# Optimization experiments

Measured on AMD Instinct MI355X. Metric: run time of the kernel, lower is better.

## Reference

```python
import jax, jax.numpy as jnp
import numpy as np
from jax import lax

IN_CH, OUT_CH, K, STYLE_DIM = 512, 512, 3, 512
B, H, W = 16, 64, 64
SCALE = 1.0 / np.sqrt(IN_CH * K * K).astype(np.float32)
EPS = 1e-8


def setup_inputs() -> dict:
    key = jax.random.key(0)
    k1, k2, k3, k4 = jax.random.split(key, 4)
    return {
        "x": jax.random.normal(k1, (B, IN_CH, H, W), dtype=jnp.float32),
        "style": jax.random.normal(k2, (B, STYLE_DIM), dtype=jnp.float32),
        "weight": jax.random.normal(k3, (1, OUT_CH, IN_CH, K, K), dtype=jnp.float32),
        "mod_w": jax.random.normal(k4, (IN_CH, STYLE_DIM), dtype=jnp.float32) / np.sqrt(STYLE_DIM),
        "mod_b": jnp.ones((IN_CH,), dtype=jnp.float32),
    }


def reference(x, style, weight, mod_w, mod_b):
    b, cin, h, w = x.shape
    out_ch = weight.shape[1]
    k = weight.shape[-1]
    pad = k // 2
    # style projection: (B, in_channel)
    s = style @ mod_w.T + mod_b
    # modulated weight: (B, out, in, k, k)
    wmod = SCALE * weight * s[:, None, :, None, None]
    # demodulation: rsqrt of sum of squares over (in, kh, kw)
    demod = lax.rsqrt(jnp.sum(wmod * wmod, axis=(2, 3, 4)) + EPS)
    wmod = wmod * demod[:, :, None, None, None]
    # grouped conv with groups = batch
    wflat = wmod.reshape(b * out_ch, cin, k, k)
    xin = x.reshape(1, b * cin, h, w)
    out = lax.conv_general_dilated(
        xin, wflat,
        window_strides=(1, 1),
        padding=[(pad, pad), (pad, pad)],
        dimension_numbers=("NCHW", "OIHW", "NCHW"),
        feature_group_count=b,
    )
    return out.reshape(b, out_ch, h, w)
```

## Files before the change

kernel.cpp:

```cpp
#include <hip/hip_runtime.h>
#include <hip/hip_bf16.h>
#include <cstdint>
#include <cstddef>

typedef __bf16 bf16x8 __attribute__((ext_vector_type(8)));
typedef float f32x4 __attribute__((ext_vector_type(4)));

#define MOD_SCALE 1.4731391e-02f
#define EPSF 1e-8f

__global__ __launch_bounds__(512) void k_style(
    const float* __restrict__ style, const float* __restrict__ mod_w,
    const float* __restrict__ mod_b, float* __restrict__ s)
{
  __shared__ float st[512];
  const int b = blockIdx.x, i = threadIdx.x;
  st[i] = style[b*512 + i];
  __syncthreads();
  const float4* mw = (const float4*)(mod_w + (size_t)i*512);
  float acc = 0.f;
  #pragma unroll 8
  for (int j = 0; j < 128; ++j) {
    float4 v = mw[j];
    acc += v.x*st[4*j] + v.y*st[4*j+1] + v.z*st[4*j+2] + v.w*st[4*j+3];
  }
  s[b*512 + i] = acc + mod_b[i];
}

__global__ __launch_bounds__(256) void k_weight(
    const float* __restrict__ weight, float* __restrict__ w2,
    __hip_bfloat16* __restrict__ Wb)
{
  const int o = blockIdx.x, t = threadIdx.x;
  #pragma unroll
  for (int h = 0; h < 2; ++h) {
    const int i = t + h*256;
    const float* wp = weight + ((size_t)o*512 + i)*9;
    float sq = 0.f;
    #pragma unroll
    for (int kk = 0; kk < 9; ++kk) {
      float v = wp[kk];
      sq += v*v;
      Wb[((size_t)kk*512 + o)*512 + i] = __float2bfloat16(v * MOD_SCALE);
    }
    w2[(size_t)o*512 + i] = sq;
  }
}

__global__ __launch_bounds__(256) void k_demod(
    const float* __restrict__ s, const float* __restrict__ w2,
    float* __restrict__ demod)
{
  __shared__ float s2[512];
  const int b = blockIdx.x, t = threadIdx.x;
  {
    float a = s[b*512 + t];        s2[t]     = a*a;
    float c = s[b*512 + t + 256];  s2[t+256] = c*c;
  }
  __syncthreads();
  #pragma unroll
  for (int h = 0; h < 2; ++h) {
    const int o = t + h*256;
    const float4* wp = (const float4*)(w2 + (size_t)o*512);
    float acc = 0.f;
    #pragma unroll 8
    for (int j = 0; j < 128; ++j) {
      float4 v = wp[j];
      acc += v.x*s2[4*j] + v.y*s2[4*j+1] + v.z*s2[4*j+2] + v.w*s2[4*j+3];
    }
    demod[b*512 + o] = rsqrtf(MOD_SCALE*MOD_SCALE*acc + EPSF);
  }
}

__global__ __launch_bounds__(256) void k_xm(
    const float* __restrict__ x, const float* __restrict__ s,
    __hip_bfloat16* __restrict__ Xm)
{
  __shared__ __hip_bfloat16 T[64][40];
  const int bid = blockIdx.x;
  const int cb = bid & 15, y = (bid >> 4) & 63, b = bid >> 10;
  const int ic0 = cb*32;
  const int t = threadIdx.x;
  const int i = t >> 3, x0 = (t & 7)*8;
  const float sv = s[b*512 + ic0 + i];
  const float4* xp = (const float4*)(x + (size_t)(b*512 + ic0 + i)*4096 + y*64 + x0);
  float4 v0 = xp[0], v1 = xp[1];
  float vals[8] = {v0.x, v0.y, v0.z, v0.w, v1.x, v1.y, v1.z, v1.w};
  #pragma unroll
  for (int j = 0; j < 8; ++j) T[x0+j][i] = __float2bfloat16(vals[j]*sv);
  __syncthreads();
  const int p = t >> 2, c = (t & 3)*8;
  __hip_bfloat16* dst = Xm + (((size_t)(b*66 + (y+1))*66 + (p+1))*512 + ic0 + c);
  *(float4*)dst = *(const float4*)&T[p][c];
}

#define VMC(n) asm volatile("s_waitcnt vmcnt(" #n ")" ::: "memory")

__global__ __launch_bounds__(512, 2) void k_conv(
    const __hip_bfloat16* __restrict__ Wb,
    const __hip_bfloat16* __restrict__ Xm,
    const float* __restrict__ demod,
    float* __restrict__ out)
{
  __shared__ __hip_bfloat16 lds[2][2][16384];

  const int orig = blockIdx.x;
  const int swz = (orig & 7)*64 + (orig >> 3);
  const int b  = swz >> 5;
  const int nt = (swz & 31) >> 1;
  const int mt = swz & 1;
  const int o0 = mt*256, y0 = nt*4;

  const int tid = threadIdx.x;
  const int l = tid & 63;
  const int w = tid >> 6;
  const int wm = w >> 2;
  const int wn = w & 3;

  const int srow = tid >> 3;
  const int scol = ((tid & 7) << 4) ^ ((srow & 7) << 4);
  const char* WbC = (const char*)Wb;
  const char* XmC = (const char*)Xm;

  const int frow = l & 15;
  const int fk0 = ((l >> 4) << 4) ^ ((l & 7) << 4);
  const int fk1 = fk0 ^ 64;
  const int aRow0 = (wm*64 + frow)*128;
  const int bRow0 = (wn*32 + frow)*128;

  #define STAGE_A(tau, h, bfi) do { \
    const int kk_ = (tau) >> 3; \
    const int cb_ = ((tau) & 7) << 7; \
    _Pragma("unroll") \
    for (int it_ = 0; it_ < 2; ++it_) { \
      const int orow_ = o0 + (h)*128 + it_*64 + srow; \
      const char* src_ = WbC + (size_t)(kk_*512 + orow_)*1024 + cb_ + scol; \
      __builtin_amdgcn_global_load_lds( \
        (__attribute__((address_space(1))) void*)src_, \
        (__attribute__((address_space(3))) void*)((char*)&lds[bfi][0][0] + (h)*16384 + it_*8192 + w*1024), \
        16, 0, 0); \
    } \
  } while(0)

  #define STAGE_B(tau, h, bfi) do { \
    const int kk_ = (tau) >> 3; \
    const int cb_ = ((tau) & 7) << 7; \
    const int dy_ = kk_/3 - 1, dx_ = kk_ - (kk_/3)*3 - 1; \
    _Pragma("unroll") \
    for (int it_ = 0; it_ < 2; ++it_) { \
      const int py_ = y0 + (h)*2 + it_ + dy_ + 1; \
      const int px_ = srow + dx_ + 1; \
      const char* src_ = XmC + ((size_t)((b*66 + py_)*66 + px_))*1024 + cb_ + scol; \
      __builtin_amdgcn_global_load_lds( \
        (__attribute__((address_space(1))) void*)src_, \
        (__attribute__((address_space(3))) void*)((char*)&lds[bfi][1][0] + (h)*16384 + it_*8192 + w*1024), \
        16, 0, 0); \
    } \
  } while(0)

  #define RD_A(Ab, MH) do { \
    _Pragma("unroll") \
    for (int mi_ = 0; mi_ < 4; ++mi_) { \
      a_[mi_][0] = *(const bf16x8*)((Ab) + aRow0 + (MH)*16384 + mi_*2048 + fk0); \
      a_[mi_][1] = *(const bf16x8*)((Ab) + aRow0 + (MH)*16384 + mi_*2048 + fk1); \
    } \
  } while(0)

  #define RD_B(Bb, NH) do { \
    _Pragma("unroll") \
    for (int ni_ = 0; ni_ < 2; ++ni_) { \
      b_[ni_][0] = *(const bf16x8*)((Bb) + bRow0 + (NH)*16384 + ni_*2048 + fk0); \
      b_[ni_][1] = *(const bf16x8*)((Bb) + bRow0 + (NH)*16384 + ni_*2048 + fk1); \
    } \
  } while(0)

  #define MFMAQ(MH, NH) do { \
    _Pragma("unroll") \
    for (int mi_ = 0; mi_ < 4; ++mi_) \
      _Pragma("unroll") \
      for (int ni_ = 0; ni_ < 2; ++ni_) { \
        acc[(MH)*4+mi_][(NH)*2+ni_] = __builtin_amdgcn_mfma_f32_16x16x32_bf16( \
            a_[mi_][0], b_[ni_][0], acc[(MH)*4+mi_][(NH)*2+ni_], 0, 0, 0); \
        acc[(MH)*4+mi_][(NH)*2+ni_] = __builtin_amdgcn_mfma_f32_16x16x32_bf16( \
            a_[mi_][1], b_[ni_][1], acc[(MH)*4+mi_][(NH)*2+ni_], 0, 0, 0); \
      } \
  } while(0)

  #define TILE(BFI, S1, S2, S3, S4, VM2, VM4) do { \
    const char* Ab_ = (const char*)&lds[BFI][0][0]; \
    const char* Bb_ = (const char*)&lds[BFI][1][0]; \
    bf16x8 a_[4][2], b_[2][2]; \
     \
    RD_A(Ab_, 0); RD_B(Bb_, 0); \
    S1; \
    __builtin_amdgcn_s_barrier(); \
    __builtin_amdgcn_s_setprio(1); MFMAQ(0, 0); __builtin_amdgcn_s_setprio(0); \
    __builtin_amdgcn_s_barrier(); \
     \
    RD_A(Ab_, 1); \
    S2; \
    __builtin_amdgcn_s_barrier(); \
    __builtin_amdgcn_s_setprio(1); MFMAQ(1, 0); __builtin_amdgcn_s_setprio(0); \
    VM2; \
    __builtin_amdgcn_s_barrier(); \
     \
    RD_B(Bb_, 1); \
    S3; \
    __builtin_amdgcn_s_barrier(); \
    __builtin_amdgcn_s_setprio(1); MFMAQ(1, 1); __builtin_amdgcn_s_setprio(0); \
    __builtin_amdgcn_s_barrier(); \
     \
    RD_A(Ab_, 0); \
    S4; \
    __builtin_amdgcn_s_barrier(); \
    __builtin_amdgcn_s_setprio(1); MFMAQ(0, 1); __builtin_amdgcn_s_setprio(0); \
    VM4; \
    __builtin_amdgcn_s_barrier(); \
  } while(0)

  f32x4 acc[8][4] = {};

  STAGE_A(0, 0, 0); STAGE_A(0, 1, 0); STAGE_B(0, 0, 0); STAGE_B(0, 1, 0);
  STAGE_B(1, 0, 1); STAGE_A(1, 1, 1);
  VMC(4);
  __builtin_amdgcn_s_barrier();

  #pragma unroll 1
  for (int tt = 0; tt < 35; ++tt) {
    const int t = tt*2;
    TILE(0, STAGE_A(t+1,0,1), STAGE_B(t+1,1,1), STAGE_B(t+2,0,0), STAGE_A(t+2,1,0),
            VMC(8), VMC(6));
    TILE(1, STAGE_A(t+2,0,0), STAGE_B(t+2,1,0), STAGE_B(t+3,0,1), STAGE_A(t+3,1,1),
            VMC(8), VMC(6));
  }
  TILE(0, STAGE_A(71,0,1), STAGE_B(71,1,1), (void)0, (void)0, VMC(8), VMC(2));
  TILE(1, (void)0, (void)0, (void)0, (void)0, VMC(0), (void)0);

  #pragma unroll
  for (int m = 0; m < 8; ++m) {
    const int o = o0 + wm*64 + (m >> 2)*128 + (m & 3)*16 + ((l >> 4) << 2);
    const f32x4 dm = *(const f32x4*)(demod + b*512 + o);
    #pragma unroll
    for (int n = 0; n < 4; ++n) {
      const int nc = wn*32 + (n >> 1)*128 + (n & 1)*16 + (l & 15);
      const int y = y0 + (nc >> 6), xx = nc & 63;
      float* op = out + (size_t)(b*512 + o)*4096 + y*64 + xx;
      #pragma unroll
      for (int r = 0; r < 4; ++r)
        op[(size_t)r*4096] = acc[m][n][r]*dm[r];
    }
  }
  #undef TILE
  #undef MFMAQ
  #undef RD_A
  #undef RD_B
  #undef STAGE_A
  #undef STAGE_B
}

extern "C" void kernel_launch(void* const* d_in, const int* in_sizes, int n_in,
                              void* d_out, int out_size, void* d_ws, size_t ws_size,
                              hipStream_t stream)
{
  const float* x      = (const float*)d_in[0];
  const float* style  = (const float*)d_in[1];
  const float* weight = (const float*)d_in[2];
  const float* mod_w  = (const float*)d_in[3];
  const float* mod_b  = (const float*)d_in[4];
  float* out = (float*)d_out;

  char* ws = (char*)d_ws;
  float* s            = (float*)(ws);
  float* demod        = (float*)(ws + 32768);
  float* w2           = (float*)(ws + 65536);
  __hip_bfloat16* Wb  = (__hip_bfloat16*)(ws + 1114112);
  __hip_bfloat16* Xm  = (__hip_bfloat16*)(ws + 5832704);

  hipMemsetAsync(Xm, 0, (size_t)16*66*66*512*2, stream);

  k_style <<<16,    512, 0, stream>>>(style, mod_w, mod_b, s);
  k_weight<<<512,   256, 0, stream>>>(weight, w2, Wb);
  k_demod <<<16,    256, 0, stream>>>(s, w2, demod);
  k_xm    <<<16384, 256, 0, stream>>>(x, s, Xm);
  k_conv  <<<512,   512, 0, stream>>>(Wb, Xm, demod, out);
}
```

Before: 397.1 us.

## Switch conv MFMA to 32x32x16 tiles and zero Xm halo in k_xm

```diff
diff --git a/kernel.cpp b/kernel.cpp
--- a/kernel.cpp
+++ b/kernel.cpp
@@ -5,6 +5,7 @@
 
 typedef __bf16 bf16x8 __attribute__((ext_vector_type(8)));
 typedef float f32x4 __attribute__((ext_vector_type(4)));
+typedef float f32x16 __attribute__((ext_vector_type(16)));
 
 #define MOD_SCALE 1.4731391e-02f
 #define EPSF 1e-8f
@@ -88,6 +89,28 @@
   float vals[8] = {v0.x, v0.y, v0.z, v0.w, v1.x, v1.y, v1.z, v1.w};
   #pragma unroll
   for (int j = 0; j < 8; ++j) T[x0+j][i] = __float2bfloat16(vals[j]*sv);
+
+  const float4 z4 = make_float4(0.f, 0.f, 0.f, 0.f);
+  if (t < 8) {
+    const int side = t >> 2, j = t & 3;
+    float4* hz = (float4*)(Xm + (((size_t)(b*66 + (y+1))*66 + side*65)*512 + ic0 + j*8));
+    *hz = z4;
+  }
+  if (y == 0) {
+    for (int idx = t; idx < 264; idx += 256) {
+      const int px = idx >> 2, j = idx & 3;
+      float4* hz = (float4*)(Xm + (((size_t)(b*66 + 0)*66 + px)*512 + ic0 + j*8));
+      *hz = z4;
+    }
+  }
+  if (y == 63) {
+    for (int idx = t; idx < 264; idx += 256) {
+      const int px = idx >> 2, j = idx & 3;
+      float4* hz = (float4*)(Xm + (((size_t)(b*66 + 65)*66 + px)*512 + ic0 + j*8));
+      *hz = z4;
+    }
+  }
+
   __syncthreads();
   const int p = t >> 2, c = (t & 3)*8;
   __hip_bfloat16* dst = Xm + (((size_t)(b*66 + (y+1))*66 + (p+1))*512 + ic0 + c);
@@ -122,11 +145,11 @@
   const char* WbC = (const char*)Wb;
   const char* XmC = (const char*)Xm;
 
-  const int frow = l & 15;
-  const int fk0 = ((l >> 4) << 4) ^ ((l & 7) << 4);
-  const int fk1 = fk0 ^ 64;
-  const int aRow0 = (wm*64 + frow)*128;
-  const int bRow0 = (wn*32 + frow)*128;
+  const int lr = l & 31;
+  const int sB = (l & 7) << 4;
+  const int kx = (l >> 5) << 4;
+  const int aBase = (wm*64 + lr)*128;
+  const int bBase = (wn*32 + lr)*128;
 
   #define STAGE_A(tau, h, bfi) do { \
     const int kk_ = (tau) >> 3; \
@@ -158,67 +181,61 @@
     } \
   } while(0)
 
-  #define RD_A(Ab, MH) do { \
-    _Pragma("unroll") \
-    for (int mi_ = 0; mi_ < 4; ++mi_) { \
-      a_[mi_][0] = *(const bf16x8*)((Ab) + aRow0 + (MH)*16384 + mi_*2048 + fk0); \
-      a_[mi_][1] = *(const bf16x8*)((Ab) + aRow0 + (MH)*16384 + mi_*2048 + fk1); \
-    } \
-  } while(0)
-
-  #define RD_B(Bb, NH) do { \
-    _Pragma("unroll") \
-    for (int ni_ = 0; ni_ < 2; ++ni_) { \
-      b_[ni_][0] = *(const bf16x8*)((Bb) + bRow0 + (NH)*16384 + ni_*2048 + fk0); \
-      b_[ni_][1] = *(const bf16x8*)((Bb) + bRow0 + (NH)*16384 + ni_*2048 + fk1); \
-    } \
-  } while(0)
-
-  #define MFMAQ(MH, NH) do { \
-    _Pragma("unroll") \
-    for (int mi_ = 0; mi_ < 4; ++mi_) \
+  #define RD_A(Ab, MH, dst) do { \
+    _Pragma("unroll") \
+    for (int mi_ = 0; mi_ < 2; ++mi_) \
       _Pragma("unroll") \
-      for (int ni_ = 0; ni_ < 2; ++ni_) { \
-        acc[(MH)*4+mi_][(NH)*2+ni_] = __builtin_amdgcn_mfma_f32_16x16x32_bf16( \
-            a_[mi_][0], b_[ni_][0], acc[(MH)*4+mi_][(NH)*2+ni_], 0, 0, 0); \
-        acc[(MH)*4+mi_][(NH)*2+ni_] = __builtin_amdgcn_mfma_f32_16x16x32_bf16( \
-            a_[mi_][1], b_[ni_][1], acc[(MH)*4+mi_][(NH)*2+ni_], 0, 0, 0); \
-      } \
-  } while(0)
-
-  #define TILE(BFI, S1, S2, S3, S4, VM2, VM4) do { \
+      for (int ks_ = 0; ks_ < 4; ++ks_) \
+        dst[mi_][ks_] = *(const bf16x8*)((Ab) + (MH)*16384 + mi_*4096 + aBase + ((ks_*32 + kx) ^ sB)); \
+  } while(0)
+
+  #define RD_B(Bb, NH, dst) do { \
+    _Pragma("unroll") \
+    for (int ks_ = 0; ks_ < 4; ++ks_) \
+      dst[ks_] = *(const bf16x8*)((Bb) + (NH)*16384 + bBase + ((ks_*32 + kx) ^ sB)); \
+  } while(0)
+
+  #define MFMAQ(AM0, dstA, NH, dstB) do { \
+    _Pragma("unroll") \
+    for (int mi_ = 0; mi_ < 2; ++mi_) \
+      _Pragma("unroll") \
+      for (int ks_ = 0; ks_ < 4; ++ks_) \
+        acc[(AM0)+mi_][NH] = __builtin_amdgcn_mfma_f32_32x32x16_bf16( \
+            dstA[mi_][ks_], dstB[ks_], acc[(AM0)+mi_][NH], 0, 0, 0); \
+  } while(0)
+
+  #define TILE(BFI, S1, S2, S3, S4, VM1, VM4) do { \
     const char* Ab_ = (const char*)&lds[BFI][0][0]; \
     const char* Bb_ = (const char*)&lds[BFI][1][0]; \
-    bf16x8 a_[4][2], b_[2][2]; \
+    bf16x8 a0_[2][4], a1_[2][4], b0_[4], b1_[4]; \
      \
-    RD_A(Ab_, 0); RD_B(Bb_, 0); \
+    RD_A(Ab_, 0, a0_); RD_B(Bb_, 0, b0_); \
     S1; \
     __builtin_amdgcn_s_barrier(); \
-    __builtin_amdgcn_s_setprio(1); MFMAQ(0, 0); __builtin_amdgcn_s_setprio(0); \
+    __builtin_amdgcn_s_setprio(1); MFMAQ(0, a0_, 0, b0_); __builtin_amdgcn_s_setprio(0); \
+    VM1; \
     __builtin_amdgcn_s_barrier(); \
      \
-    RD_A(Ab_, 1); \
+    RD_B(Bb_, 1, b1_); \
     S2; \
     __builtin_amdgcn_s_barrier(); \
-    __builtin_amdgcn_s_setprio(1); MFMAQ(1, 0); __builtin_amdgcn_s_setprio(0); \
-    VM2; \
+    __builtin_amdgcn_s_setprio(1); MFMAQ(0, a0_, 1, b1_); __builtin_amdgcn_s_setprio(0); \
     __builtin_amdgcn_s_barrier(); \
      \
-    RD_B(Bb_, 1); \
+    RD_A(Ab_, 1, a1_); \
     S3; \
     __builtin_amdgcn_s_barrier(); \
-    __builtin_amdgcn_s_setprio(1); MFMAQ(1, 1); __builtin_amdgcn_s_setprio(0); \
+    __builtin_amdgcn_s_setprio(1); MFMAQ(2, a1_, 1, b1_); __builtin_amdgcn_s_setprio(0); \
     __builtin_amdgcn_s_barrier(); \
      \
-    RD_A(Ab_, 0); \
     S4; \
     __builtin_amdgcn_s_barrier(); \
-    __builtin_amdgcn_s_setprio(1); MFMAQ(0, 1); __builtin_amdgcn_s_setprio(0); \
+    __builtin_amdgcn_s_setprio(1); MFMAQ(2, a1_, 0, b0_); __builtin_amdgcn_s_setprio(0); \
     VM4; \
     __builtin_amdgcn_s_barrier(); \
   } while(0)
 
-  f32x4 acc[8][4] = {};
+  f32x16 acc[4][2] = {};
 
   STAGE_A(0, 0, 0); STAGE_A(0, 1, 0); STAGE_B(0, 0, 0); STAGE_B(0, 1, 0);
   STAGE_B(1, 0, 1); STAGE_A(1, 1, 1);
@@ -229,25 +246,28 @@
   for (int tt = 0; tt < 35; ++tt) {
     const int t = tt*2;
     TILE(0, STAGE_A(t+1,0,1), STAGE_B(t+1,1,1), STAGE_B(t+2,0,0), STAGE_A(t+2,1,0),
-            VMC(8), VMC(6));
+            VMC(6), VMC(6));
     TILE(1, STAGE_A(t+2,0,0), STAGE_B(t+2,1,0), STAGE_B(t+3,0,1), STAGE_A(t+3,1,1),
-            VMC(8), VMC(6));
-  }
-  TILE(0, STAGE_A(71,0,1), STAGE_B(71,1,1), (void)0, (void)0, VMC(8), VMC(2));
+            VMC(6), VMC(6));
+  }
+  TILE(0, STAGE_A(71,0,1), STAGE_B(71,1,1), (void)0, (void)0, VMC(6), VMC(2));
   TILE(1, (void)0, (void)0, (void)0, (void)0, VMC(0), (void)0);
 
   #pragma unroll
-  for (int m = 0; m < 8; ++m) {
-    const int o = o0 + wm*64 + (m >> 2)*128 + (m & 3)*16 + ((l >> 4) << 2);
-    const f32x4 dm = *(const f32x4*)(demod + b*512 + o);
+  for (int am = 0; am < 4; ++am) {
+    const int om = o0 + (am >> 1)*128 + wm*64 + (am & 1)*32 + ((l >> 5) << 2);
     #pragma unroll
-    for (int n = 0; n < 4; ++n) {
-      const int nc = wn*32 + (n >> 1)*128 + (n & 1)*16 + (l & 15);
+    for (int NH = 0; NH < 2; ++NH) {
+      const int nc = NH*128 + wn*32 + lr;
       const int y = y0 + (nc >> 6), xx = nc & 63;
-      float* op = out + (size_t)(b*512 + o)*4096 + y*64 + xx;
       #pragma unroll
-      for (int r = 0; r < 4; ++r)
-        op[(size_t)r*4096] = acc[m][n][r]*dm[r];
+      for (int g = 0; g < 4; ++g) {
+        const f32x4 dm = *(const f32x4*)(demod + b*512 + om + 8*g);
+        float* op = out + (size_t)(b*512 + om + 8*g)*4096 + y*64 + xx;
+        #pragma unroll
+        for (int j = 0; j < 4; ++j)
+          op[(size_t)j*4096] = acc[am][NH][g*4 + j] * dm[j];
+      }
     }
   }
   #undef TILE
@@ -276,8 +296,6 @@
   __hip_bfloat16* Wb  = (__hip_bfloat16*)(ws + 1114112);
   __hip_bfloat16* Xm  = (__hip_bfloat16*)(ws + 5832704);
 
-  hipMemsetAsync(Xm, 0, (size_t)16*66*66*512*2, stream);
-
   k_style <<<16,    512, 0, stream>>>(style, mod_w, mod_b, s);
   k_weight<<<512,   256, 0, stream>>>(weight, w2, Wb);
   k_demod <<<16,    256, 0, stream>>>(s, w2, demod);
```

Result: no change. 402.7 us (+1.4%).
